# Kernel tuning notes

Measured on AMD Instinct MI355X. Metric: run time of the kernel, lower is better.

Reference implementation:

```python
import jax, jax.numpy as jnp
import numpy as np

CR = 4; D = 768; H = 12; DH = 64; L = 3; I = 3072
W1S = 128  # one-sided sliding window = config.attention_window(256) // 2 (transformers convention)
MAXPOS = 7200; MLP = 512; NCLS = 3
EPS = 1e-12

def layer_norm(x, s, b):
    m = jnp.mean(x, -1, keepdims=True)
    v = jnp.var(x, -1, keepdims=True)
    return (x - m) * jax.lax.rsqrt(v + EPS) * s + b

def band_attention(q, k, v, w):
    # q,k,v: [B,H,S,dh]; each token attends to +-w neighbors (Longformer sliding chunks, no global tokens)
    B, Hh, S, dh = q.shape
    nc = S // w
    qc = q.reshape(B, Hh, nc, w, dh)
    kp = jnp.pad(k, ((0, 0), (0, 0), (w, w), (0, 0)))
    vp = jnp.pad(v, ((0, 0), (0, 0), (w, w), (0, 0)))
    idx = jnp.arange(nc)[:, None] * w + jnp.arange(3 * w)[None, :]          # [nc, 3w]
    kc = kp[:, :, idx]                                                      # [B,H,nc,3w,dh]
    vc = vp[:, :, idx]
    scores = jnp.einsum('bhcqd,bhckd->bhcqk', qc, kc) / np.float32(np.sqrt(dh))
    rel = jnp.arange(3 * w)[None, :] - w - jnp.arange(w)[:, None]           # [w,3w] key_pos - query_pos
    kpos = jnp.arange(nc)[:, None, None] * w + jnp.arange(3 * w)[None, None, :] - w
    mask = (jnp.abs(rel)[None] <= w) & (kpos >= 0) & (kpos < S)             # [nc,w,3w]
    scores = jnp.where(mask[None, None], scores, jnp.float32(-1e9))
    probs = jax.nn.softmax(scores, axis=-1)
    out = jnp.einsum('bhcqk,bhckd->bhcqd', probs, vc)
    return out.reshape(B, Hh, S, dh)

def forward(x, proj_w, proj_b, pos_emb, tok_emb, emb_ln_s, emb_ln_b,
            wq, bq, wk, bk, wv, bv, wo, bo, ln1_s, ln1_b,
            wi, bi, wo2, bo2, ln2_s, ln2_b,
            pool_w, pool_b, head_ln_s, head_ln_b, head_w1, head_b1, head_w2, head_b2):
    n, c, t, wd, hh = x.shape
    tc, sc = t // CR, wd // CR
    # torch unfold(dim, size, step) with size==step == contiguous block reshape
    xr = x[:, :, :tc * CR].reshape(n, c, CR, tc, CR, sc, CR, sc)
    xr = xr.transpose(0, 1, 2, 4, 6, 3, 5, 7)            # n,c,cr_t,cr_w,cr_h,tc,sc,sc
    xr = xr.reshape(n, c, CR ** 3, tc * sc * sc)
    xr = xr.transpose(0, 3, 2, 1).reshape(n, tc * sc * sc, CR ** 3 * c)
    h = xr @ proj_w + proj_b                             # [B,S,D]
    B, S = h.shape[0], h.shape[1]
    pos_ids = jnp.arange(S) % (MAXPOS - 2)               # no padding: S is already a multiple of 2w
    h = h + pos_emb[pos_ids][None] + tok_emb[0][None, None]
    h = layer_norm(h, emb_ln_s, emb_ln_b)
    for l in range(L):
        q = (h @ wq[l] + bq[l]).reshape(B, S, H, DH).transpose(0, 2, 1, 3)
        k = (h @ wk[l] + bk[l]).reshape(B, S, H, DH).transpose(0, 2, 1, 3)
        v = (h @ wv[l] + bv[l]).reshape(B, S, H, DH).transpose(0, 2, 1, 3)
        a = band_attention(q, k, v, W1S).transpose(0, 2, 1, 3).reshape(B, S, D)
        h = layer_norm(h + a @ wo[l] + bo[l], ln1_s[l], ln1_b[l])
        f = jax.nn.gelu(h @ wi[l] + bi[l], approximate=False) @ wo2[l] + bo2[l]
        h = layer_norm(h + f, ln2_s[l], ln2_b[l])
    pooled = jnp.tanh(h[:, 0] @ pool_w + pool_b)         # LongformerPooler on first token
    z = layer_norm(pooled, head_ln_s, head_ln_b)
    z = jax.nn.gelu(z @ head_w1 + head_b1, approximate=False)
    return z @ head_w2 + head_b2                         # [B, num_classes]

def setup_inputs() -> dict:
    key = jax.random.key(0)
    ks = iter(jax.random.split(key, 40))
    p = lambda *s: jax.random.normal(next(ks), s, jnp.float32) * 0.02
    d = {
        'x': jax.random.normal(next(ks), (8, 3, 64, 32, 32), jnp.float32),
        'position_ids': jnp.tile(jnp.arange(1024, dtype=jnp.int32)[None], (8, 1)),
        'proj_w': p(3 * CR ** 3, D), 'proj_b': p(D),
        'pos_emb': p(MAXPOS, D), 'tok_emb': p(2, D),
        'emb_ln_s': jnp.ones((D,), jnp.float32), 'emb_ln_b': jnp.zeros((D,), jnp.float32),
        'wq': p(L, D, D), 'bq': p(L, D), 'wk': p(L, D, D), 'bk': p(L, D),
        'wv': p(L, D, D), 'bv': p(L, D), 'wo': p(L, D, D), 'bo': p(L, D),
        'ln1_s': jnp.ones((L, D), jnp.float32), 'ln1_b': jnp.zeros((L, D), jnp.float32),
        'wi': p(L, D, I), 'bi': p(L, I), 'wo2': p(L, I, D), 'bo2': p(L, D),
        'ln2_s': jnp.ones((L, D), jnp.float32), 'ln2_b': jnp.zeros((L, D), jnp.float32),
        'pool_w': p(D, D), 'pool_b': p(D),
        'head_ln_s': jnp.ones((D,), jnp.float32), 'head_ln_b': jnp.zeros((D,), jnp.float32),
        'head_w1': p(D, MLP), 'head_b1': p(MLP),
        'head_w2': p(MLP, NCLS), 'head_b2': p(NCLS),
    }
    return d

def reference(x, position_ids, proj_w, proj_b, pos_emb, tok_emb, emb_ln_s, emb_ln_b,
              wq, bq, wk, bk, wv, bv, wo, bo, ln1_s, ln1_b,
              wi, bi, wo2, bo2, ln2_s, ln2_b,
              pool_w, pool_b, head_ln_s, head_ln_b, head_w1, head_b1, head_w2, head_b2):
    # position_ids is overwritten inside the spat_temp branch of the original forward (arange over cuboids)
    return forward(x, proj_w, proj_b, pos_emb, tok_emb, emb_ln_s, emb_ln_b,
                   wq, bq, wk, bk, wv, bv, wo, bo, ln1_s, ln1_b,
                   wi, bi, wo2, bo2, ln2_s, ln2_b,
                   pool_w, pool_b, head_ln_s, head_ln_b, head_w1, head_b1, head_w2, head_b2)
```

## Files before the change

kernel.cpp:

```cpp
#include <hip/hip_runtime.h>
#include <hip/hip_bf16.h>
#include <math.h>


typedef __attribute__((ext_vector_type(8))) short short8;
typedef __attribute__((ext_vector_type(4))) short short4v;
typedef __attribute__((ext_vector_type(4))) float floatx4;

__device__ __forceinline__ float gelu_exact(float x) {
    float ax = fabsf(x) * 0.70710678118654752440f;
    float t  = 1.f / (1.f + 0.3275911f * ax);
    float y  = t * (0.254829592f + t * (-0.284496736f + t * (1.421413741f +
               t * (-1.453152027f + t * 1.061405429f))));
    float erfv = copysignf(1.f - y * __expf(-ax * ax), x);
    return 0.5f * x * (1.f + erfv);
}

__device__ __forceinline__ short bfs(float x) {
    __hip_bfloat16 h = __float2bfloat16(x);
    short s;
    __builtin_memcpy(&s, &h, 2);
    return s;
}

__device__ __forceinline__ float bf2f(short s) {
    unsigned u = ((unsigned)(unsigned short)s) << 16;
    float f;
    __builtin_memcpy(&f, &u, 4);
    return f;
}

#define GLOAD_LDS16(g, l) __builtin_amdgcn_global_load_lds( \
    (const __attribute__((address_space(1))) void*)(g),     \
    (__attribute__((address_space(3))) void*)(l), 16, 0, 0)

__global__ __launch_bounds__(256) void weight_prep(
    const float* __restrict__ wq, const float* __restrict__ wk,
    const float* __restrict__ wv, const float* __restrict__ wo,
    const float* __restrict__ wi, const float* __restrict__ wo2,
    const float* __restrict__ pj, const float* __restrict__ pw,
    const float* __restrict__ h1,
    const float* __restrict__ bq, const float* __restrict__ bk,
    const float* __restrict__ bv,
    __hip_bfloat16* __restrict__ qkvw_t, __hip_bfloat16* __restrict__ wo_t,
    __hip_bfloat16* __restrict__ wi_t, __hip_bfloat16* __restrict__ wo2_t,
    __hip_bfloat16* __restrict__ projw_t, __hip_bfloat16* __restrict__ poolw_t,
    __hip_bfloat16* __restrict__ w1_t, float* __restrict__ qkv_b)
{
    int gid = blockIdx.x;
    if (gid >= 21840) {
        int idx = (gid - 21840) * 256 + threadIdx.x;
        if (idx < 6912) {
            int l = idx / 2304, r = idx - l * 2304;
            float v = (r < 768) ? bq[l * 768 + r]
                    : (r < 1536) ? bk[l * 768 + r - 768]
                                 : bv[l * 768 + r - 1536];
            qkv_b[idx] = v;
        }
        return;
    }
    const float* W; __hip_bfloat16* Wt;
    int K, N, tx, tpl, local;
    long inLS, outLS;
    if (gid < 6912) {
        int j = gid / 1728; local = gid - j * 1728;
        K = 768; N = 768; tx = 24; tpl = 576; inLS = 589824;
        if      (j == 0) { W = wq; Wt = qkvw_t;           outLS = 1769472; }
        else if (j == 1) { W = wk; Wt = qkvw_t + 589824;  outLS = 1769472; }
        else if (j == 2) { W = wv; Wt = qkvw_t + 1179648; outLS = 1769472; }
        else             { W = wo; Wt = wo_t;             outLS = 589824;  }
    } else if (gid < 13824) {
        local = gid - 6912;  W = wi;  Wt = wi_t;
        K = 768; N = 3072; tx = 96; tpl = 2304; inLS = 2359296; outLS = 2359296;
    } else if (gid < 20736) {
        local = gid - 13824; W = wo2; Wt = wo2_t;
        K = 3072; N = 768; tx = 24; tpl = 2304; inLS = 2359296; outLS = 2359296;
    } else if (gid < 20880) {
        local = gid - 20736; W = pj;  Wt = projw_t;
        K = 192; N = 768; tx = 24; tpl = 144; inLS = 0; outLS = 0;
    } else if (gid < 21456) {
        local = gid - 20880; W = pw;  Wt = poolw_t;
        K = 768; N = 768; tx = 24; tpl = 576; inLS = 0; outLS = 0;
    } else {
        local = gid - 21456; W = h1;  Wt = w1_t;
        K = 768; N = 512; tx = 16; tpl = 384; inLS = 0; outLS = 0;
    }
    int l   = local / tpl;
    int rem = local - l * tpl;
    int bx = rem % tx, by = rem / tx;
    __shared__ float tile[32][33];
    const float* Wl = W + (long)l * inLS;
    __hip_bfloat16* Wtl = Wt + (long)l * outLS;
    int lx = threadIdx.x & 31, ly = threadIdx.x >> 5;
    int kb = by * 32, nb = bx * 32;
    #pragma unroll
    for (int r = 0; r < 32; r += 8)
        tile[ly + r][lx] = Wl[(long)(kb + ly + r) * N + nb + lx];
    __syncthreads();
    #pragma unroll
    for (int r = 0; r < 32; r += 8)
        Wtl[(long)(nb + ly + r) * K + kb + lx] = __float2bfloat16(tile[lx][ly + r]);
}

__global__ __launch_bounds__(192) void gather_x(
    const float* __restrict__ x, __hip_bfloat16* __restrict__ xr)
{
    int tok = blockIdx.x;
    int b = tok >> 10, s = tok & 1023;
    int tci = s >> 6, sci = (s >> 3) & 7, scj = s & 7;
    int f = threadIdx.x;
    int ch  = f % 3;
    int crc = f / 3;
    int cr1 = crc >> 4, cr2 = (crc >> 2) & 3, cr3 = crc & 3;
    float v = x[(((b * 3 + ch) * 64) + cr1 * 16 + tci) * 1024 +
                (cr2 * 8 + sci) * 32 + cr3 * 8 + scj];
    xr[(long)tok * 192 + f] = __float2bfloat16(v);
}

template<int ACT>
__global__ __launch_bounds__(256, 4) void mfma_gemm(
    const __hip_bfloat16* __restrict__ A, const __hip_bfloat16* __restrict__ Bt,
    const float* __restrict__ bias, __hip_bfloat16* __restrict__ C,
    int M, int N, int K)
{
    __shared__ short lds_raw[32768];
    short* LB = lds_raw;
    int tid  = threadIdx.x;
    int wave = tid >> 6, lane = tid & 63;
    int L = blockIdx.x;
    long m0 = (long)(L & 63) * 128, n0 = (long)(L >> 6) * 128;
    int wr = wave >> 1, wc = wave & 1;
    floatx4 acc[4][4] = {};

    int srow = (wave * 128 + lane) >> 2;
    int sch  = (lane & 3) ^ ((lane >> 3) & 3);
    const __hip_bfloat16* Ag = A  + (m0 + srow) * K + sch * 8;
    const __hip_bfloat16* Bg = Bt + (n0 + srow) * K + sch * 8;
    int lm = lane & 15, lg = lane >> 4;
    int lk8 = ((lg ^ ((lm >> 1) & 3))) * 8;

    auto stage = [&](int buf, int k0) {
        short* a0 = LB + buf * 8192 + wave * 1024;
        short* a1 = a0 + 4096;
        short* b0 = LB + 16384 + buf * 8192 + wave * 1024;
        short* b1 = b0 + 4096;
        GLOAD_LDS16(Ag + k0,               a0);
        GLOAD_LDS16(Ag + 16 * K + k0,      a0 + 512);
        GLOAD_LDS16(Ag + k0 + 32,          a1);
        GLOAD_LDS16(Ag + 16 * K + k0 + 32, a1 + 512);
        GLOAD_LDS16(Bg + k0,               b0);
        GLOAD_LDS16(Bg + 16 * K + k0,      b0 + 512);
        GLOAD_LDS16(Bg + k0 + 32,          b1);
        GLOAD_LDS16(Bg + 16 * K + k0 + 32, b1 + 512);
    };

    stage(0, 0);
    int buf = 0;
    for (int k0 = 0; k0 < K; k0 += 64, buf ^= 1) {
        __syncthreads();
        if (k0 + 64 < K) stage(buf ^ 1, k0 + 64);
        #pragma unroll
        for (int c = 0; c < 2; c++) {
            const __hip_bfloat16* Ab =
                (const __hip_bfloat16*)(LB + buf * 8192 + c * 4096);
            const __hip_bfloat16* Bb =
                (const __hip_bfloat16*)(LB + 16384 + buf * 8192 + c * 4096);
            short8 af[4];
            #pragma unroll
            for (int mi = 0; mi < 4; mi++)
                af[mi] = *(const short8*)&Ab[(wr * 64 + mi * 16 + lm) * 32 + lk8];
            #pragma unroll
            for (int ni = 0; ni < 4; ni++) {
                short8 bf = *(const short8*)&Bb[(wc * 64 + ni * 16 + lm) * 32 + lk8];
                #pragma unroll
                for (int mi = 0; mi < 4; mi++)
                    acc[mi][ni] = __builtin_amdgcn_mfma_f32_16x16x32_bf16(
                        af[mi], bf, acc[mi][ni], 0, 0, 0);
            }
        }
    }
    __syncthreads();

    float bvv[4];
    #pragma unroll
    for (int ni = 0; ni < 4; ni++)
        bvv[ni] = bias[n0 + wc * 64 + ni * 16 + lm];
    int erow = tid >> 4;
    int ecol = (tid & 15) * 8;
    #pragma unroll
    for (int p = 0; p < 2; p++) {
        if (wr == p) {
            #pragma unroll
            for (int mi = 0; mi < 4; mi++)
                #pragma unroll
                for (int ni = 0; ni < 4; ni++)
                    #pragma unroll
                    for (int j = 0; j < 4; j++) {
                        float o = acc[mi][ni][j] + bvv[ni];
                        if (ACT == 1) o = gelu_exact(o);
                        lds_raw[(mi * 16 + lg * 4 + j) * 136 +
                                wc * 64 + ni * 16 + lm] = bfs(o);
                    }
        }
        __syncthreads();
        #pragma unroll
        for (int rr = 0; rr < 4; rr++) {
            int r = erow + rr * 16;
            short8 v = *(const short8*)&lds_raw[r * 136 + ecol];
            *(short8*)&C[(m0 + p * 64 + r) * N + n0 + ecol] = v;
        }
        __syncthreads();
    }
}

__global__ __launch_bounds__(192) void pos_ln_kernel(
    const __hip_bfloat16* __restrict__ t, const float* __restrict__ pos_emb,
    const float* __restrict__ tok_emb, const float* __restrict__ ln_s,
    const float* __restrict__ ln_b, float* __restrict__ h,
    __hip_bfloat16* __restrict__ hbf)
{
    int tok = blockIdx.x;
    int s = tok & 1023;
    int tid = threadIdx.x;
    int d = tid * 4;
    __shared__ float red[6];
    short4v tv = *(const short4v*)&t[(long)tok * 768 + d];
    float4 pv = *(const float4*)&pos_emb[s * 768 + d];
    float4 kv = *(const float4*)&tok_emb[d];
    float a[4] = { bf2f(tv[0]) + pv.x + kv.x, bf2f(tv[1]) + pv.y + kv.y,
                   bf2f(tv[2]) + pv.z + kv.z, bf2f(tv[3]) + pv.w + kv.w };
    float sum = a[0] + a[1] + a[2] + a[3];
    float sumsq = a[0]*a[0] + a[1]*a[1] + a[2]*a[2] + a[3]*a[3];
    #pragma unroll
    for (int off = 32; off; off >>= 1) {
        sum   += __shfl_down(sum, off, 64);
        sumsq += __shfl_down(sumsq, off, 64);
    }
    if ((tid & 63) == 0) { red[tid >> 6] = sum; red[3 + (tid >> 6)] = sumsq; }
    __syncthreads();
    sum   = red[0] + red[1] + red[2];
    sumsq = red[3] + red[4] + red[5];
    float mean = sum * (1.f / 768.f);
    float var  = sumsq * (1.f / 768.f) - mean * mean;
    float rs   = rsqrtf(var + 1e-12f);
    float4 sv = *(const float4*)&ln_s[d];
    float4 bv = *(const float4*)&ln_b[d];
    float4 o;
    o.x = (a[0] - mean) * rs * sv.x + bv.x;
    o.y = (a[1] - mean) * rs * sv.y + bv.y;
    o.z = (a[2] - mean) * rs * sv.z + bv.z;
    o.w = (a[3] - mean) * rs * sv.w + bv.w;
    *(float4*)&h[(long)tok * 768 + d] = o;
    short4v ob = { bfs(o.x), bfs(o.y), bfs(o.z), bfs(o.w) };
    *(short4v*)&hbf[(long)tok * 768 + d] = ob;
}

__global__ __launch_bounds__(256) void attn_kernel(
    const __hip_bfloat16* __restrict__ QKV, __hip_bfloat16* __restrict__ Ob)
{
    __shared__ __hip_bfloat16 KV[128 * 72];
    __shared__ __hip_bfloat16 Pl[4][32 * 136];
    __shared__ float alpha_s[4][32];
    __shared__ float l_s[4][32];

    int blk = blockIdx.x;
    int ci = blk & 7, hh = (blk >> 3) % 12, b = blk / 96;
    int tid = threadIdx.x, w = tid >> 6, lane = tid & 63;
    int lm = lane & 15, lg = lane >> 4;
    __hip_bfloat16* Pw = &Pl[w][0];

    short8 qf[2][2];
    #pragma unroll
    for (int nt = 0; nt < 2; nt++) {
        int q = ci * 128 + w * 32 + nt * 16 + lm;
        const __hip_bfloat16* qp = &QKV[((long)(b * 1024 + q)) * 2304 + hh * 64];
        #pragma unroll
        for (int ks = 0; ks < 2; ks++)
            qf[nt][ks] = *(const short8*)(qp + ks * 32 + lg * 8);
    }

    floatx4 accO[2][4] = {};
    float m_run[2] = {-1e30f, -1e30f};
    float l_run[2] = {0.f, 0.f};

    for (int tt = 0; tt < 3; tt++) {
        __syncthreads();
        #pragma unroll
        for (int i = 0; i < 4; i++) {
            int e = tid + i * 256;
            int jj = e >> 3, dd = (e & 7) * 8;
            int kpos = ci * 128 + tt * 128 + jj - 128;
            short8 kv = {};
            if (kpos >= 0 && kpos < 1024)
                kv = *(const short8*)&QKV[((long)(b * 1024 + kpos)) * 2304 + 768 + hh * 64 + dd];
            *(short8*)&KV[jj * 72 + dd] = kv;
        }
        __syncthreads();

        floatx4 accS[8][2] = {};
        #pragma unroll
        for (int ks = 0; ks < 2; ks++)
            #pragma unroll
            for (int mt = 0; mt < 8; mt++) {
                short8 kf = *(const short8*)&KV[(mt * 16 + lm) * 72 + ks * 32 + lg * 8];
                accS[mt][0] = __builtin_amdgcn_mfma_f32_16x16x32_bf16(kf, qf[0][ks], accS[mt][0], 0, 0, 0);
                accS[mt][1] = __builtin_amdgcn_mfma_f32_16x16x32_bf16(kf, qf[1][ks], accS[mt][1], 0, 0, 0);
            }

        float tmax[2] = {-1e30f, -1e30f};
        #pragma unroll
        for (int nt = 0; nt < 2; nt++) {
            int r = w * 32 + nt * 16 + lm;
            #pragma unroll
            for (int mt = 0; mt < 8; mt++)
                #pragma unroll
                for (int j = 0; j < 4; j++) {
                    int jrel = tt * 128 + mt * 16 + lg * 4 + j;
                    int kpos = ci * 128 + jrel - 128;
                    bool valid = (jrel >= r) && (jrel <= r + 256) &&
                                 (kpos >= 0) && (kpos < 1024);
                    float s = valid ? accS[mt][nt][j] * 0.125f : -1e9f;
                    accS[mt][nt][j] = s;
                    tmax[nt] = fmaxf(tmax[nt], s);
                }
            tmax[nt] = fmaxf(tmax[nt], __shfl_xor(tmax[nt], 16));
            tmax[nt] = fmaxf(tmax[nt], __shfl_xor(tmax[nt], 32));
        }

        float al[2];
        #pragma unroll
        for (int nt = 0; nt < 2; nt++) {
            float mnew = fmaxf(m_run[nt], tmax[nt]);
            al[nt] = __expf(m_run[nt] - mnew);
            m_run[nt] = mnew;
            float ts = 0.f;
            #pragma unroll
            for (int mt = 0; mt < 8; mt++) {
                short4v pp;
                #pragma unroll
                for (int j = 0; j < 4; j++) {
                    float p = __expf(accS[mt][nt][j] - mnew);
                    ts += p;
                    pp[j] = bfs(p);
                }
                *(short4v*)&Pw[(nt * 16 + lm) * 136 + mt * 16 + lg * 4] = pp;
            }
            ts += __shfl_xor(ts, 16);
            ts += __shfl_xor(ts, 32);
            l_run[nt] = l_run[nt] * al[nt] + ts;
        }
        if (lg < 2) alpha_s[w][lg * 16 + lm] = al[lg];

        __syncthreads();
        #pragma unroll
        for (int i = 0; i < 4; i++) {
            int e = tid + i * 256;
            int jj = e >> 3, dd = (e & 7) * 8;
            int kpos = ci * 128 + tt * 128 + jj - 128;
            short8 vv = {};
            if (kpos >= 0 && kpos < 1024)
                vv = *(const short8*)&QKV[((long)(b * 1024 + kpos)) * 2304 + 1536 + hh * 64 + dd];
            short* kvs = (short*)KV;
            #pragma unroll
            for (int m2 = 0; m2 < 8; m2++)
                kvs[(dd + m2) * 136 + jj] = vv[m2];
        }
        __syncthreads();

        #pragma unroll
        for (int mo = 0; mo < 2; mo++)
            #pragma unroll
            for (int j = 0; j < 4; j++) {
                float a = alpha_s[w][mo * 16 + lg * 4 + j];
                #pragma unroll
                for (int nd = 0; nd < 4; nd++)
                    accO[mo][nd][j] *= a;
            }

        #pragma unroll
        for (int kk = 0; kk < 4; kk++) {
            short8 pf[2], vf[4];
            #pragma unroll
            for (int mo = 0; mo < 2; mo++)
                pf[mo] = *(const short8*)&Pw[(mo * 16 + lm) * 136 + kk * 32 + lg * 8];
            #pragma unroll
            for (int nd = 0; nd < 4; nd++)
                vf[nd] = *(const short8*)&KV[(nd * 16 + lm) * 136 + kk * 32 + lg * 8];
            #pragma unroll
            for (int mo = 0; mo < 2; mo++)
                #pragma unroll
                for (int nd = 0; nd < 4; nd++)
                    accO[mo][nd] = __builtin_amdgcn_mfma_f32_16x16x32_bf16(
                        pf[mo], vf[nd], accO[mo][nd], 0, 0, 0);
        }
    }

    if (lg < 2) l_s[w][lg * 16 + lm] = l_run[lg];
    #pragma unroll
    for (int mo = 0; mo < 2; mo++)
        #pragma unroll
        for (int j = 0; j < 4; j++) {
            int qr = mo * 16 + lg * 4 + j;
            float rl = 1.f / l_s[w][qr];
            int q  = w * 32 + qr;
            long base = ((long)(b * 1024 + ci * 128 + q)) * 768 + hh * 64;
            #pragma unroll
            for (int nd = 0; nd < 4; nd++)
                Ob[base + nd * 16 + lm] = __float2bfloat16(accO[mo][nd][j] * rl);
        }
}

__global__ __launch_bounds__(192) void add_ln_kernel(
    float* __restrict__ h, const __hip_bfloat16* __restrict__ t,
    const float* __restrict__ ln_s, const float* __restrict__ ln_b,
    __hip_bfloat16* __restrict__ hbf)
{
    int tok = blockIdx.x;
    int tid = threadIdx.x;
    int d = tid * 4;
    __shared__ float red[6];
    float* hrow = &h[(long)tok * 768];
    float4 hv = *(const float4*)&hrow[d];
    short4v tv = *(const short4v*)&t[(long)tok * 768 + d];
    float a[4] = { hv.x + bf2f(tv[0]), hv.y + bf2f(tv[1]),
                   hv.z + bf2f(tv[2]), hv.w + bf2f(tv[3]) };
    float sum = a[0] + a[1] + a[2] + a[3];
    float sumsq = a[0]*a[0] + a[1]*a[1] + a[2]*a[2] + a[3]*a[3];
    #pragma unroll
    for (int off = 32; off; off >>= 1) {
        sum   += __shfl_down(sum, off, 64);
        sumsq += __shfl_down(sumsq, off, 64);
    }
    if ((tid & 63) == 0) { red[tid >> 6] = sum; red[3 + (tid >> 6)] = sumsq; }
    __syncthreads();
    sum   = red[0] + red[1] + red[2];
    sumsq = red[3] + red[4] + red[5];
    float mean = sum * (1.f / 768.f);
    float var  = sumsq * (1.f / 768.f) - mean * mean;
    float rs   = rsqrtf(var + 1e-12f);
    float4 sv = *(const float4*)&ln_s[d];
    float4 bv = *(const float4*)&ln_b[d];
    float4 o;
    o.x = (a[0] - mean) * rs * sv.x + bv.x;
    o.y = (a[1] - mean) * rs * sv.y + bv.y;
    o.z = (a[2] - mean) * rs * sv.z + bv.z;
    o.w = (a[3] - mean) * rs * sv.w + bv.w;
    *(float4*)&hrow[d] = o;
    short4v ob = { bfs(o.x), bfs(o.y), bfs(o.z), bfs(o.w) };
    *(short4v*)&hbf[(long)tok * 768 + d] = ob;
}

__global__ __launch_bounds__(256) void pool_split(
    const __hip_bfloat16* __restrict__ hbf, const __hip_bfloat16* __restrict__ pool_wt,
    const float* __restrict__ pool_b, float* __restrict__ pooled)
{
    int g = blockIdx.x * 256 + threadIdx.x;
    int out = g >> 3, t8 = g & 7;
    int b = out / 768, d = out - b * 768;
    const __hip_bfloat16* hr = hbf + (long)b * 1024 * 768;
    const __hip_bfloat16* wr = pool_wt + (long)d * 768;
    float acc = 0.f;
    #pragma unroll
    for (int kk = 0; kk < 96; kk += 8) {
        int k = t8 * 96 + kk;
        short8 hv = *(const short8*)&hr[k];
        short8 wv = *(const short8*)&wr[k];
        #pragma unroll
        for (int j = 0; j < 8; j++) acc += bf2f(hv[j]) * bf2f(wv[j]);
    }
    acc += __shfl_down(acc, 4, 64);
    acc += __shfl_down(acc, 2, 64);
    acc += __shfl_down(acc, 1, 64);
    if (t8 == 0) pooled[out] = tanhf(acc + pool_b[d]);
}

__global__ __launch_bounds__(256) void ln_z_kernel(
    const float* __restrict__ pooled, const float* __restrict__ hln_s,
    const float* __restrict__ hln_b, __hip_bfloat16* __restrict__ zbf)
{
    int b = blockIdx.x, tid = threadIdx.x;
    __shared__ float red[8];
    const float* pr = &pooled[b * 768];
    float p0 = pr[tid], p1 = pr[tid + 256], p2 = pr[tid + 512];
    float sum = p0 + p1 + p2;
    float sumsq = p0 * p0 + p1 * p1 + p2 * p2;
    #pragma unroll
    for (int off = 32; off; off >>= 1) {
        sum   += __shfl_down(sum, off, 64);
        sumsq += __shfl_down(sumsq, off, 64);
    }
    if ((tid & 63) == 0) { red[tid >> 6] = sum; red[4 + (tid >> 6)] = sumsq; }
    __syncthreads();
    sum   = red[0] + red[1] + red[2] + red[3];
    sumsq = red[4] + red[5] + red[6] + red[7];
    float mean = sum * (1.f / 768.f);
    float var  = sumsq * (1.f / 768.f) - mean * mean;
    float rs   = rsqrtf(var + 1e-12f);
    zbf[b * 768 + tid]       = __float2bfloat16((p0 - mean) * rs * hln_s[tid]       + hln_b[tid]);
    zbf[b * 768 + tid + 256] = __float2bfloat16((p1 - mean) * rs * hln_s[tid + 256] + hln_b[tid + 256]);
    zbf[b * 768 + tid + 512] = __float2bfloat16((p2 - mean) * rs * hln_s[tid + 512] + hln_b[tid + 512]);
}

__global__ __launch_bounds__(256) void mlp_split(
    const __hip_bfloat16* __restrict__ zbf, const __hip_bfloat16* __restrict__ w1t,
    const float* __restrict__ b1, float* __restrict__ z1)
{
    int g = blockIdx.x * 256 + threadIdx.x;
    int out = g >> 3, t8 = g & 7;
    int b = out >> 9, d = out & 511;
    const __hip_bfloat16* zr = zbf + b * 768;
    const __hip_bfloat16* wr = w1t + (long)d * 768;
    float acc = 0.f;
    #pragma unroll
    for (int kk = 0; kk < 96; kk += 8) {
        int k = t8 * 96 + kk;
        short8 zv = *(const short8*)&zr[k];
        short8 wv = *(const short8*)&wr[k];
        #pragma unroll
        for (int j = 0; j < 8; j++) acc += bf2f(zv[j]) * bf2f(wv[j]);
    }
    acc += __shfl_down(acc, 4, 64);
    acc += __shfl_down(acc, 2, 64);
    acc += __shfl_down(acc, 1, 64);
    if (t8 == 0) z1[out] = gelu_exact(acc + b1[d]);
}

__global__ __launch_bounds__(256) void head_final_kernel(
    const float* __restrict__ z1, const float* __restrict__ w2,
    const float* __restrict__ b2, float* __restrict__ out)
{
    int tid = threadIdx.x;
    int g = tid >> 3, t8 = tid & 7;
    if (g < 24) {
        int b = g / 3, o = g % 3;
        float acc = 0.f;
        for (int k = t8; k < 512; k += 8)
            acc += z1[b * 512 + k] * w2[k * 3 + o];
        acc += __shfl_down(acc, 4, 64);
        acc += __shfl_down(acc, 2, 64);
        acc += __shfl_down(acc, 1, 64);
        if (t8 == 0) out[b * 3 + o] = acc + b2[o];
    }
}

extern "C" void kernel_launch(void* const* d_in, const int* in_sizes, int n_in,
                              void* d_out, int out_size, void* d_ws, size_t ws_size,
                              hipStream_t stream) {
    const float* x       = (const float*)d_in[0];
    const float* proj_w  = (const float*)d_in[2];
    const float* proj_b  = (const float*)d_in[3];
    const float* pos_emb = (const float*)d_in[4];
    const float* tok_emb = (const float*)d_in[5];
    const float* eln_s   = (const float*)d_in[6];
    const float* eln_b   = (const float*)d_in[7];
    const float* wq      = (const float*)d_in[8];
    const float* bq      = (const float*)d_in[9];
    const float* wk      = (const float*)d_in[10];
    const float* bk      = (const float*)d_in[11];
    const float* wv      = (const float*)d_in[12];
    const float* bv      = (const float*)d_in[13];
    const float* wo      = (const float*)d_in[14];
    const float* bo      = (const float*)d_in[15];
    const float* ln1_s   = (const float*)d_in[16];
    const float* ln1_b   = (const float*)d_in[17];
    const float* wi      = (const float*)d_in[18];
    const float* bi      = (const float*)d_in[19];
    const float* wo2     = (const float*)d_in[20];
    const float* bo2     = (const float*)d_in[21];
    const float* ln2_s   = (const float*)d_in[22];
    const float* ln2_b   = (const float*)d_in[23];
    const float* pool_w  = (const float*)d_in[24];
    const float* pool_b  = (const float*)d_in[25];
    const float* hln_s   = (const float*)d_in[26];
    const float* hln_b   = (const float*)d_in[27];
    const float* hw1     = (const float*)d_in[28];
    const float* hb1     = (const float*)d_in[29];
    const float* hw2     = (const float*)d_in[30];
    const float* hb2     = (const float*)d_in[31];

    char* wp = (char*)d_ws;
    auto alloc = [&](size_t bytes) {
        char* p = wp; wp += (bytes + 255) & ~(size_t)255; return p;
    };
    float*          h       = (float*)alloc(8192ll * 768 * 4);
    __hip_bfloat16* qkv_bf  = (__hip_bfloat16*)alloc(8192ll * 2304 * 2);
    __hip_bfloat16* t_bf    = (__hip_bfloat16*)alloc(8192ll * 768 * 2);
    __hip_bfloat16* mlp_bf  = (__hip_bfloat16*)alloc(8192ll * 3072 * 2);
    __hip_bfloat16* h_bf    = (__hip_bfloat16*)alloc(8192ll * 768 * 2);
    __hip_bfloat16* a_bf    = (__hip_bfloat16*)alloc(8192ll * 768 * 2);
    __hip_bfloat16* qkvw_t  = (__hip_bfloat16*)alloc(3ll * 2304 * 768 * 2);
    __hip_bfloat16* wo_t    = (__hip_bfloat16*)alloc(3ll * 768 * 768 * 2);
    __hip_bfloat16* wi_t    = (__hip_bfloat16*)alloc(3ll * 3072 * 768 * 2);
    __hip_bfloat16* wo2_t   = (__hip_bfloat16*)alloc(3ll * 768 * 3072 * 2);
    float*          qkv_b   = (float*)alloc(3ll * 2304 * 4);
    __hip_bfloat16* xr_bf   = (__hip_bfloat16*)alloc(8192ll * 192 * 2);
    __hip_bfloat16* projw_t = (__hip_bfloat16*)alloc(768ll * 192 * 2);
    __hip_bfloat16* poolw_t = (__hip_bfloat16*)alloc(768ll * 768 * 2);
    __hip_bfloat16* w1_t    = (__hip_bfloat16*)alloc(512ll * 768 * 2);
    float*          pooled  = (float*)alloc(8ll * 768 * 4);
    __hip_bfloat16* z_bf    = (__hip_bfloat16*)alloc(8ll * 768 * 2);
    float*          z1      = (float*)alloc(8ll * 512 * 4);

    weight_prep<<<21867, 256, 0, stream>>>(
        wq, wk, wv, wo, wi, wo2, proj_w, pool_w, hw1, bq, bk, bv,
        qkvw_t, wo_t, wi_t, wo2_t, projw_t, poolw_t, w1_t, qkv_b);

    gather_x<<<8192, 192, 0, stream>>>(x, xr_bf);
    mfma_gemm<0><<<6 * 64, 256, 0, stream>>>(
        xr_bf, projw_t, proj_b, t_bf, 8192, 768, 192);
    pos_ln_kernel<<<8192, 192, 0, stream>>>(t_bf, pos_emb, tok_emb, eln_s, eln_b, h, h_bf);

    for (int l = 0; l < 3; l++) {
        mfma_gemm<0><<<18 * 64, 256, 0, stream>>>(
            h_bf, qkvw_t + (long)l * 2304 * 768, qkv_b + l * 2304, qkv_bf,
            8192, 2304, 768);
        attn_kernel<<<768, 256, 0, stream>>>(qkv_bf, a_bf);
        mfma_gemm<0><<<6 * 64, 256, 0, stream>>>(
            a_bf, wo_t + (long)l * 768 * 768, bo + l * 768, t_bf,
            8192, 768, 768);
        add_ln_kernel<<<8192, 192, 0, stream>>>(h, t_bf, ln1_s + l * 768, ln1_b + l * 768, h_bf);
        mfma_gemm<1><<<24 * 64, 256, 0, stream>>>(
            h_bf, wi_t + (long)l * 3072 * 768, bi + l * 3072, mlp_bf,
            8192, 3072, 768);
        mfma_gemm<0><<<6 * 64, 256, 0, stream>>>(
            mlp_bf, wo2_t + (long)l * 768 * 3072, bo2 + l * 768, t_bf,
            8192, 768, 3072);
        add_ln_kernel<<<8192, 192, 0, stream>>>(h, t_bf, ln2_s + l * 768, ln2_b + l * 768, h_bf);
    }

    pool_split<<<192, 256, 0, stream>>>(h_bf, poolw_t, pool_b, pooled);
    ln_z_kernel<<<8, 256, 0, stream>>>(pooled, hln_s, hln_b, z_bf);
    mlp_split<<<128, 256, 0, stream>>>(z_bf, w1_t, hb1, z1);
    head_final_kernel<<<1, 256, 0, stream>>>(z1, hw2, hb2, (float*)d_out);
}
```

Baseline: 1.048 ms.

## Skip fully masked attention tiles, merge gather into prep, fuse classifier head

```diff
diff --git a/kernel.cpp b/kernel.cpp
--- a/kernel.cpp
+++ b/kernel.cpp
@@ -42,12 +42,27 @@
     const float* __restrict__ h1,
     const float* __restrict__ bq, const float* __restrict__ bk,
     const float* __restrict__ bv,
+    const float* __restrict__ x,
     __hip_bfloat16* __restrict__ qkvw_t, __hip_bfloat16* __restrict__ wo_t,
     __hip_bfloat16* __restrict__ wi_t, __hip_bfloat16* __restrict__ wo2_t,
     __hip_bfloat16* __restrict__ projw_t, __hip_bfloat16* __restrict__ poolw_t,
-    __hip_bfloat16* __restrict__ w1_t, float* __restrict__ qkv_b)
+    __hip_bfloat16* __restrict__ w1_t, float* __restrict__ qkv_b,
+    __hip_bfloat16* __restrict__ xr)
 {
     int gid = blockIdx.x;
+    if (gid >= 21867) {
+        int idx = (gid - 21867) * 256 + threadIdx.x;
+        int tok = idx / 192, f = idx - tok * 192;
+        int b = tok >> 10, s = tok & 1023;
+        int tci = s >> 6, sci = (s >> 3) & 7, scj = s & 7;
+        int ch  = f % 3;
+        int crc = f / 3;
+        int cr1 = crc >> 4, cr2 = (crc >> 2) & 3, cr3 = crc & 3;
+        float v = x[(((b * 3 + ch) * 64) + cr1 * 16 + tci) * 1024 +
+                    (cr2 * 8 + sci) * 32 + cr3 * 8 + scj];
+        xr[(long)tok * 192 + f] = __float2bfloat16(v);
+        return;
+    }
     if (gid >= 21840) {
         int idx = (gid - 21840) * 256 + threadIdx.x;
         if (idx < 6912) {
@@ -102,21 +117,6 @@
         Wtl[(long)(nb + ly + r) * K + kb + lx] = __float2bfloat16(tile[lx][ly + r]);
 }
 
-__global__ __launch_bounds__(192) void gather_x(
-    const float* __restrict__ x, __hip_bfloat16* __restrict__ xr)
-{
-    int tok = blockIdx.x;
-    int b = tok >> 10, s = tok & 1023;
-    int tci = s >> 6, sci = (s >> 3) & 7, scj = s & 7;
-    int f = threadIdx.x;
-    int ch  = f % 3;
-    int crc = f / 3;
-    int cr1 = crc >> 4, cr2 = (crc >> 2) & 3, cr3 = crc & 3;
-    float v = x[(((b * 3 + ch) * 64) + cr1 * 16 + tci) * 1024 +
-                (cr2 * 8 + sci) * 32 + cr3 * 8 + scj];
-    xr[(long)tok * 192 + f] = __float2bfloat16(v);
-}
-
 template<int ACT>
 __global__ __launch_bounds__(256, 4) void mfma_gemm(
     const __hip_bfloat16* __restrict__ A, const __hip_bfloat16* __restrict__ Bt,
@@ -284,6 +284,7 @@
     float l_run[2] = {0.f, 0.f};
 
     for (int tt = 0; tt < 3; tt++) {
+        if ((tt == 0 && ci == 0) || (tt == 2 && ci == 7)) continue;
         __syncthreads();
         #pragma unroll
         for (int i = 0; i < 4; i++) {
@@ -302,6 +303,8 @@
         for (int ks = 0; ks < 2; ks++)
             #pragma unroll
             for (int mt = 0; mt < 8; mt++) {
+                if ((tt == 0 && mt < 2 * w) || (tt == 2 && mt >= 2 * w + 2))
+                    continue;
                 short8 kf = *(const short8*)&KV[(mt * 16 + lm) * 72 + ks * 32 + lg * 8];
                 accS[mt][0] = __builtin_amdgcn_mfma_f32_16x16x32_bf16(kf, qf[0][ks], accS[mt][0], 0, 0, 0);
                 accS[mt][1] = __builtin_amdgcn_mfma_f32_16x16x32_bf16(kf, qf[1][ks], accS[mt][1], 0, 0, 0);
@@ -312,7 +315,9 @@
         for (int nt = 0; nt < 2; nt++) {
             int r = w * 32 + nt * 16 + lm;
             #pragma unroll
-            for (int mt = 0; mt < 8; mt++)
+            for (int mt = 0; mt < 8; mt++) {
+                if ((tt == 0 && mt < 2 * w) || (tt == 2 && mt >= 2 * w + 2))
+                    continue;
                 #pragma unroll
                 for (int j = 0; j < 4; j++) {
                     int jrel = tt * 128 + mt * 16 + lg * 4 + j;
@@ -323,6 +328,7 @@
                     accS[mt][nt][j] = s;
                     tmax[nt] = fmaxf(tmax[nt], s);
                 }
+            }
             tmax[nt] = fmaxf(tmax[nt], __shfl_xor(tmax[nt], 16));
             tmax[nt] = fmaxf(tmax[nt], __shfl_xor(tmax[nt], 32));
         }
@@ -336,6 +342,8 @@
             float ts = 0.f;
             #pragma unroll
             for (int mt = 0; mt < 8; mt++) {
+                if ((tt == 0 && mt < 2 * w) || (tt == 2 && mt >= 2 * w + 2))
+                    continue;
                 short4v pp;
                 #pragma unroll
                 for (int j = 0; j < 4; j++) {
@@ -379,6 +387,8 @@
 
         #pragma unroll
         for (int kk = 0; kk < 4; kk++) {
+            if ((tt == 0 && kk < w) || (tt == 2 && kk > w))
+                continue;
             short8 pf[2], vf[4];
             #pragma unroll
             for (int mo = 0; mo < 2; mo++)
@@ -450,38 +460,39 @@
     *(short4v*)&hbf[(long)tok * 768 + d] = ob;
 }
 
-__global__ __launch_bounds__(256) void pool_split(
-    const __hip_bfloat16* __restrict__ hbf, const __hip_bfloat16* __restrict__ pool_wt,
-    const float* __restrict__ pool_b, float* __restrict__ pooled)
+__global__ __launch_bounds__(256) void head_fused(
+    const __hip_bfloat16* __restrict__ hbf,
+    const __hip_bfloat16* __restrict__ pool_wt, const float* __restrict__ pool_b,
+    const float* __restrict__ hln_s, const float* __restrict__ hln_b,
+    const __hip_bfloat16* __restrict__ w1t, const float* __restrict__ b1,
+    const float* __restrict__ w2, const float* __restrict__ b2,
+    float* __restrict__ out)
 {
-    int g = blockIdx.x * 256 + threadIdx.x;
-    int out = g >> 3, t8 = g & 7;
-    int b = out / 768, d = out - b * 768;
+    __shared__ __hip_bfloat16 hrow[768];
+    __shared__ float pooled[768];
+    __shared__ float red[8];
+    __shared__ __hip_bfloat16 zrow[768];
+    __shared__ float z1s[512];
+    int b = blockIdx.x, tid = threadIdx.x;
     const __hip_bfloat16* hr = hbf + (long)b * 1024 * 768;
-    const __hip_bfloat16* wr = pool_wt + (long)d * 768;
-    float acc = 0.f;
-    #pragma unroll
-    for (int kk = 0; kk < 96; kk += 8) {
-        int k = t8 * 96 + kk;
-        short8 hv = *(const short8*)&hr[k];
-        short8 wv = *(const short8*)&wr[k];
-        #pragma unroll
-        for (int j = 0; j < 8; j++) acc += bf2f(hv[j]) * bf2f(wv[j]);
-    }
-    acc += __shfl_down(acc, 4, 64);
-    acc += __shfl_down(acc, 2, 64);
-    acc += __shfl_down(acc, 1, 64);
-    if (t8 == 0) pooled[out] = tanhf(acc + pool_b[d]);
-}
-
-__global__ __launch_bounds__(256) void ln_z_kernel(
-    const float* __restrict__ pooled, const float* __restrict__ hln_s,
-    const float* __restrict__ hln_b, __hip_bfloat16* __restrict__ zbf)
-{
-    int b = blockIdx.x, tid = threadIdx.x;
-    __shared__ float red[8];
-    const float* pr = &pooled[b * 768];
-    float p0 = pr[tid], p1 = pr[tid + 256], p2 = pr[tid + 512];
+    #pragma unroll
+    for (int r = 0; r < 3; r++) hrow[tid + r * 256] = hr[tid + r * 256];
+    __syncthreads();
+    #pragma unroll
+    for (int rep = 0; rep < 3; rep++) {
+        int d = tid + rep * 256;
+        const __hip_bfloat16* wr = pool_wt + (long)d * 768;
+        float acc = 0.f;
+        for (int k = 0; k < 768; k += 8) {
+            short8 hv = *(const short8*)&hrow[k];
+            short8 wv = *(const short8*)&wr[k];
+            #pragma unroll
+            for (int j = 0; j < 8; j++) acc += bf2f(hv[j]) * bf2f(wv[j]);
+        }
+        pooled[d] = tanhf(acc + pool_b[d]);
+    }
+    __syncthreads();
+    float p0 = pooled[tid], p1 = pooled[tid + 256], p2 = pooled[tid + 512];
     float sum = p0 + p1 + p2;
     float sumsq = p0 * p0 + p1 * p1 + p2 * p2;
     #pragma unroll
@@ -496,50 +507,28 @@
     float mean = sum * (1.f / 768.f);
     float var  = sumsq * (1.f / 768.f) - mean * mean;
     float rs   = rsqrtf(var + 1e-12f);
-    zbf[b * 768 + tid]       = __float2bfloat16((p0 - mean) * rs * hln_s[tid]       + hln_b[tid]);
-    zbf[b * 768 + tid + 256] = __float2bfloat16((p1 - mean) * rs * hln_s[tid + 256] + hln_b[tid + 256]);
-    zbf[b * 768 + tid + 512] = __float2bfloat16((p2 - mean) * rs * hln_s[tid + 512] + hln_b[tid + 512]);
-}
-
-__global__ __launch_bounds__(256) void mlp_split(
-    const __hip_bfloat16* __restrict__ zbf, const __hip_bfloat16* __restrict__ w1t,
-    const float* __restrict__ b1, float* __restrict__ z1)
-{
-    int g = blockIdx.x * 256 + threadIdx.x;
-    int out = g >> 3, t8 = g & 7;
-    int b = out >> 9, d = out & 511;
-    const __hip_bfloat16* zr = zbf + b * 768;
-    const __hip_bfloat16* wr = w1t + (long)d * 768;
-    float acc = 0.f;
-    #pragma unroll
-    for (int kk = 0; kk < 96; kk += 8) {
-        int k = t8 * 96 + kk;
-        short8 zv = *(const short8*)&zr[k];
-        short8 wv = *(const short8*)&wr[k];
-        #pragma unroll
-        for (int j = 0; j < 8; j++) acc += bf2f(zv[j]) * bf2f(wv[j]);
-    }
-    acc += __shfl_down(acc, 4, 64);
-    acc += __shfl_down(acc, 2, 64);
-    acc += __shfl_down(acc, 1, 64);
-    if (t8 == 0) z1[out] = gelu_exact(acc + b1[d]);
-}
-
-__global__ __launch_bounds__(256) void head_final_kernel(
-    const float* __restrict__ z1, const float* __restrict__ w2,
-    const float* __restrict__ b2, float* __restrict__ out)
-{
-    int tid = threadIdx.x;
-    int g = tid >> 3, t8 = tid & 7;
-    if (g < 24) {
-        int b = g / 3, o = g % 3;
+    zrow[tid]       = __float2bfloat16((p0 - mean) * rs * hln_s[tid]       + hln_b[tid]);
+    zrow[tid + 256] = __float2bfloat16((p1 - mean) * rs * hln_s[tid + 256] + hln_b[tid + 256]);
+    zrow[tid + 512] = __float2bfloat16((p2 - mean) * rs * hln_s[tid + 512] + hln_b[tid + 512]);
+    __syncthreads();
+    #pragma unroll
+    for (int rep = 0; rep < 2; rep++) {
+        int d = tid + rep * 256;
+        const __hip_bfloat16* wr = w1t + (long)d * 768;
         float acc = 0.f;
-        for (int k = t8; k < 512; k += 8)
-            acc += z1[b * 512 + k] * w2[k * 3 + o];
-        acc += __shfl_down(acc, 4, 64);
-        acc += __shfl_down(acc, 2, 64);
-        acc += __shfl_down(acc, 1, 64);
-        if (t8 == 0) out[b * 3 + o] = acc + b2[o];
+        for (int k = 0; k < 768; k += 8) {
+            short8 zv = *(const short8*)&zrow[k];
+            short8 wv = *(const short8*)&wr[k];
+            #pragma unroll
+            for (int j = 0; j < 8; j++) acc += bf2f(zv[j]) * bf2f(wv[j]);
+        }
+        z1s[d] = gelu_exact(acc + b1[d]);
+    }
+    __syncthreads();
+    if (tid < 3) {
+        float acc = 0.f;
+        for (int k = 0; k < 512; k++) acc += z1s[k] * w2[k * 3 + tid];
+        out[b * 3 + tid] = acc + b2[tid];
     }
 }
 
@@ -597,15 +586,11 @@
     __hip_bfloat16* projw_t = (__hip_bfloat16*)alloc(768ll * 192 * 2);
     __hip_bfloat16* poolw_t = (__hip_bfloat16*)alloc(768ll * 768 * 2);
     __hip_bfloat16* w1_t    = (__hip_bfloat16*)alloc(512ll * 768 * 2);
-    float*          pooled  = (float*)alloc(8ll * 768 * 4);
-    __hip_bfloat16* z_bf    = (__hip_bfloat16*)alloc(8ll * 768 * 2);
-    float*          z1      = (float*)alloc(8ll * 512 * 4);
-
-    weight_prep<<<21867, 256, 0, stream>>>(
-        wq, wk, wv, wo, wi, wo2, proj_w, pool_w, hw1, bq, bk, bv,
-        qkvw_t, wo_t, wi_t, wo2_t, projw_t, poolw_t, w1_t, qkv_b);
-
-    gather_x<<<8192, 192, 0, stream>>>(x, xr_bf);
+
+    weight_prep<<<28011, 256, 0, stream>>>(
+        wq, wk, wv, wo, wi, wo2, proj_w, pool_w, hw1, bq, bk, bv, x,
+        qkvw_t, wo_t, wi_t, wo2_t, projw_t, poolw_t, w1_t, qkv_b, xr_bf);
+
     mfma_gemm<0><<<6 * 64, 256, 0, stream>>>(
         xr_bf, projw_t, proj_b, t_bf, 8192, 768, 192);
     pos_ln_kernel<<<8192, 192, 0, stream>>>(t_bf, pos_emb, tok_emb, eln_s, eln_b, h, h_bf);
@@ -628,8 +613,6 @@
         add_ln_kernel<<<8192, 192, 0, stream>>>(h, t_bf, ln2_s + l * 768, ln2_b + l * 768, h_bf);
     }
 
-    pool_split<<<192, 256, 0, stream>>>(h_bf, poolw_t, pool_b, pooled);
-    ln_z_kernel<<<8, 256, 0, stream>>>(pooled, hln_s, hln_b, z_bf);
-    mlp_split<<<128, 256, 0, stream>>>(z_bf, w1_t, hb1, z1);
-    head_final_kernel<<<1, 256, 0, stream>>>(z1, hw2, hb2, (float*)d_out);
-}
+    head_fused<<<8, 256, 0, stream>>>(h_bf, poolw_t, pool_b, hln_s, hln_b,
+                                      w1_t, hb1, hw2, hb2, (float*)d_out);
+}
```

Measured after the change: 1.066 ms. No clear change (+1.7%).
